# Optimization experiments

Hardware: AMD Instinct MI355X
Metric: run time of the kernel (lower is better)

## Reference

```python
import jax, jax.numpy as jnp
import numpy as np

BETA = 0.25


def setup_inputs() -> dict:
    key = jax.random.key(0)
    k1, k2 = jax.random.split(key)
    x = jax.random.normal(k1, (32, 64, 64, 64), dtype=jnp.float32)   # [B, C, H, W]
    emb = jax.random.normal(k2, (1024, 64), dtype=jnp.float32)       # [K, C] codebook
    return {"x": x, "emb": emb}


def reference(x, emb):
    b, c, h, w = x.shape
    # (b h w) c
    z = jnp.transpose(x, (0, 2, 3, 1)).reshape(-1, c)
    # squared euclidean distances (argmin identical to torch.cdist argmin)
    # ||z||^2 - 2 z e^T + ||e||^2, never taking sqrt since only argmin is used
    d = (jnp.sum(z * z, axis=1, keepdims=True)
         - 2.0 * jnp.einsum('nc,kc->nk', z, emb)
         + jnp.sum(emb * emb, axis=1)[None, :])        # [N, K]
    idx = jnp.argmin(d, axis=1)                        # [N] int
    e = emb[idx]                                       # gather [N, C]
    e = jnp.transpose(e.reshape(b, h, w, c), (0, 3, 1, 2))  # [B, C, H, W]
    codebook_loss = jnp.mean((jax.lax.stop_gradient(x) - e) ** 2)
    commitment_loss = BETA * jnp.mean((x - jax.lax.stop_gradient(e)) ** 2)
    loss = codebook_loss + commitment_loss
    o = x + jax.lax.stop_gradient(e - x)               # straight-through
    indices = idx.reshape(b, h, w)
    return (o, loss, indices)
```

## Files before the change

### kernel.cpp

```cpp
#include <hip/hip_runtime.h>

#define CCH     64
#define HW      4096
#define NPIX    131072
#define KCODES  1024
#define NELEM   (NPIX * CCH)
#define PPB     512
#define HALFK   512
#define MARGIN_Q 2u

typedef _Float16 f16;
typedef __attribute__((ext_vector_type(8))) _Float16 f16x8;
typedef __attribute__((ext_vector_type(4))) float    f32x4;

static __device__ __forceinline__ f32x4 mfma16(f16x8 a, f16x8 b, f32x4 c) {
    return __builtin_amdgcn_mfma_f32_16x16x32_f16(a, b, c, 0, 0, 0);
}
static __device__ __forceinline__ unsigned med3u(unsigned a, unsigned b, unsigned c) {
    unsigned d;
    asm("v_med3_u32 %0, %1, %2, %3" : "=v"(d) : "v"(a), "v"(b), "v"(c));
    return d;
}

__global__ __launch_bounds__(512, 2) void vq_fused(
    const float* __restrict__ x, const float* __restrict__ emb,
    float* __restrict__ o, float* __restrict__ idx_out,
    float* __restrict__ partial)
{
    __shared__ __align__(16) f16 cbH[HALFK * CCH];
    __shared__ __align__(16) f16 cbL[HALFK * CCH];
    __shared__ float eebl[HALFK];
    __shared__ unsigned buS[PPB];
    __shared__ float wred[8];

    const int t    = threadIdx.x;
    const int lane = t & 63;
    const int w    = t >> 6;
    const int col  = lane & 15;
    const int quad = lane >> 4;
    const int sw0  = 8 * (quad ^ (col & 7));
    const int sw1  = sw0 ^ 32;
    const int n0   = blockIdx.x * PPB;
    const int b    = n0 >> 12;
    const int p0   = n0 & 4095;
    const float* xb = x + (size_t)b * (CCH * HW) + p0;

    f16x8 aH[4][2], aL[4][2];
#pragma unroll
    for (int rt = 0; rt < 4; ++rt) {
        const int pp = w * 64 + rt * 16 + col;
#pragma unroll
        for (int kc = 0; kc < 2; ++kc) {
            f16x8 h, l;
#pragma unroll
            for (int j = 0; j < 8; ++j) {
                const int c = kc * 32 + quad * 8 + j;
                float zs = -2.0f * xb[(size_t)c * HW + pp];
                f16 hh = (f16)zs;
                h[j] = hh;
                l[j] = (f16)(zs - (float)hh);
            }
            aH[rt][kc] = h;
            aL[rt][kc] = l;
        }
    }

    unsigned best[16], best2[16];
#pragma unroll
    for (int s = 0; s < 16; ++s) { best[s] = 0xFFFFFFFFu; best2[s] = 0xFFFFFFFFu; }

    for (int half = 0; half < 2; ++half) {
        const int kbase = half * HALFK;
        {
            const float* src = emb + (size_t)(kbase + t) * CCH;
            float s = 0.f;
#pragma unroll
            for (int g = 0; g < 8; ++g) {
                float4 v0 = *(const float4*)(src + g * 8);
                float4 v1 = *(const float4*)(src + g * 8 + 4);
                float vv[8] = {v0.x, v0.y, v0.z, v0.w, v1.x, v1.y, v1.z, v1.w};
                f16x8 h, l;
#pragma unroll
                for (int j = 0; j < 8; ++j) {
                    f16 hh = (f16)vv[j];
                    h[j] = hh;
                    l[j] = (f16)(vv[j] - (float)hh);
                    s = fmaf(vv[j], vv[j], s);
                }
                const int off = t * 64 + 8 * (g ^ (t & 7));
                *(f16x8*)&cbH[off] = h;
                *(f16x8*)&cbL[off] = l;
            }
            eebl[t] = fmaf(s, 2048.0f, 1048576.0f);
        }
        __syncthreads();

#pragma unroll 4
        for (int tile = 0; tile < HALFK / 16; ++tile) {
            const int row = tile * 16 + col;
            const f16* bh = cbH + row * 64;
            const f16* bl = cbL + row * 64;
            f16x8 bH0 = *(const f16x8*)(bh + sw0);
            f16x8 bH1 = *(const f16x8*)(bh + sw1);
            f16x8 bL0 = *(const f16x8*)(bl + sw0);
            f16x8 bL1 = *(const f16x8*)(bl + sw1);
            const float eebc = eebl[row];
            const unsigned kb = (unsigned)(kbase + row);
#pragma unroll
            for (int rt = 0; rt < 4; ++rt) {
                f32x4 a4 = {0.f, 0.f, 0.f, 0.f};
                a4 = mfma16(aH[rt][0], bH0, a4);
                a4 = mfma16(aH[rt][1], bH1, a4);
                a4 = mfma16(aL[rt][0], bH0, a4);
                a4 = mfma16(aL[rt][1], bH1, a4);
                a4 = mfma16(aH[rt][0], bL0, a4);
                a4 = mfma16(aH[rt][1], bL1, a4);
#pragma unroll
                for (int r = 0; r < 4; ++r) {
                    float uf = fmaf(a4[r], 2048.0f, eebc);
                    unsigned pk = (((unsigned)uf) << 10) | kb;
                    const int s = rt * 4 + r;
                    best2[s] = med3u(pk, best[s], best2[s]);
                    best[s]  = min(best[s], pk);
                }
            }
        }
        __syncthreads();
    }

#pragma unroll
    for (int d = 1; d < 16; d <<= 1) {
#pragma unroll
        for (int s = 0; s < 16; ++s) {
            unsigned ob  = __shfl_xor(best[s],  d, 64);
            unsigned ob2 = __shfl_xor(best2[s], d, 64);
            best2[s] = med3u(best[s], ob, min(best2[s], ob2));
            best[s]  = min(best[s], ob);
        }
    }
    if (col == 0) {
#pragma unroll
        for (int rt = 0; rt < 4; ++rt)
#pragma unroll
            for (int r = 0; r < 4; ++r) {
                const int s = rt * 4 + r;
                const unsigned bb = best[s];
                const unsigned fl =
                    (((best2[s] >> 10) - (bb >> 10)) < MARGIN_Q) ? 0x80000000u : 0u;
                buS[w * 64 + rt * 16 + quad * 4 + r] = bb | fl;
            }
    }
    __syncthreads();

    const unsigned bu = buS[t];
    const unsigned bidx = bu & 1023u;
    idx_out[n0 + t] = (float)bidx;
    float ss = 0.f;
    {
        const float4* er4 = (const float4*)(emb + (size_t)bidx * CCH);
        const float* xbt = xb + t;
        float* ob = o + (size_t)b * (CCH * HW) + p0 + t;
#pragma unroll
        for (int i = 0; i < 16; ++i) {
            float4 ev = er4[i];
            float evv[4] = {ev.x, ev.y, ev.z, ev.w};
#pragma unroll
            for (int q = 0; q < 4; ++q) {
                const int c = i * 4 + q;
                float xv = xbt[(size_t)c * HW];
                float e  = evv[q];
                ob[(size_t)c * HW] = xv + (e - xv);
                float d = xv - e;
                ss = fmaf(d, d, ss);
            }
        }
    }
    for (int off = 32; off; off >>= 1) ss += __shfl_down(ss, off, 64);

    unsigned long long flags = __ballot((bu >> 31) != 0u);
    float extra = 0.f;
    while (flags) {
        const int m = __ffsll((long long)flags) - 1;
        flags &= flags - 1;
        const int pp2 = p0 + w * 64 + m;
        const int n   = n0 + w * 64 + m;
        const float zval = x[(size_t)b * (CCH * HW) + (size_t)lane * HW + pp2];
        float zf[CCH];
#pragma unroll
        for (int c = 0; c < CCH; ++c) zf[c] = __shfl(zval, c, 64);

        double bd = 1e300; int bi = 0;
        for (int j = 0; j < 16; ++j) {
            const int k = lane * 16 + j;
            const float4* er4 = (const float4*)(emb + (size_t)k * CCH);
            double d0 = 0.0, d1 = 0.0;
#pragma unroll
            for (int i = 0; i < 16; ++i) {
                float4 ev = er4[i];
                double t0 = (double)zf[i * 4 + 0] - (double)ev.x;
                double t1 = (double)zf[i * 4 + 1] - (double)ev.y;
                double t2 = (double)zf[i * 4 + 2] - (double)ev.z;
                double t3 = (double)zf[i * 4 + 3] - (double)ev.w;
                d0 = fma(t0, t0, d0); d1 = fma(t1, t1, d1);
                d0 = fma(t2, t2, d0); d1 = fma(t3, t3, d1);
            }
            double d = d0 + d1;
            if (d < bd) { bd = d; bi = k; }
        }
        for (int dlt = 1; dlt < 64; dlt <<= 1) {
            double od = __shfl_xor(bd, dlt, 64);
            int    oi = __shfl_xor(bi, dlt, 64);
            if (od < bd || (od == bd && oi < bi)) { bd = od; bi = oi; }
        }
        const int oldi = (int)(buS[w * 64 + m] & 1023u);
        if (bi != oldi) {
            if (lane == 0) idx_out[n] = (float)bi;
            const float xv = zval;
            const float eo = emb[(size_t)oldi * CCH + lane];
            const float en = emb[(size_t)bi   * CCH + lane];
            o[(size_t)b * (CCH * HW) + (size_t)lane * HW + pp2] = xv + (en - xv);
            const float dn = xv - en, dd = xv - eo;
            float delta = dn * dn - dd * dd;
            for (int off = 32; off; off >>= 1) delta += __shfl_down(delta, off, 64);
            extra += delta;
        }
    }

    if (lane == 0) wred[w] = ss + extra;
    __syncthreads();
    if (t == 0) {
        float tot = 0.f;
#pragma unroll
        for (int i = 0; i < 8; ++i) tot += wred[i];
        partial[blockIdx.x] = tot;
    }
}

__global__ void vq_fin(const float* __restrict__ partial, float* __restrict__ loss) {
    __shared__ float r[4];
    const int t = threadIdx.x, lane = t & 63, w = t >> 6;
    float s = partial[t];
    for (int off = 32; off; off >>= 1) s += __shfl_down(s, off, 64);
    if (lane == 0) r[w] = s;
    __syncthreads();
    if (t == 0) loss[0] = 1.25f * ((r[0] + r[1]) + (r[2] + r[3])) * (1.0f / (float)NELEM);
}

extern "C" void kernel_launch(void* const* d_in, const int* in_sizes, int n_in,
                              void* d_out, int out_size, void* d_ws, size_t ws_size,
                              hipStream_t stream) {
    const float* x   = (const float*)d_in[0];
    const float* emb = (const float*)d_in[1];
    float* out = (float*)d_out;
    float* wsf = (float*)d_ws;

    float* o_out    = out;
    float* loss_out = out + NELEM;
    float* idx_out  = out + NELEM + 1;

    vq_fused<<<NPIX / PPB, PPB, 0, stream>>>(x, emb, o_out, idx_out, wsf);
    vq_fin<<<1, 256, 0, stream>>>(wsf, loss_out);
}
```

Measured before the change: 177.8 us.

## Precompute split-f16 codebook once and stream it via double-buffered LDS DMA

A new prep kernel converts the codebook to hi/lo f16 halves and squared norms once in workspace. The main kernel no longer converts the codebook per block. It now handles 128 pixels per 256-thread block and streams 64-code chunks into double-buffered LDS with global_load_lds, so the loads overlap the MFMA work. This adds a kernel launch, more blocks and a per-chunk barrier. The med3 inline asm is replaced by min/max.

```diff
diff --git a/kernel.cpp b/kernel.cpp
--- a/kernel.cpp
+++ b/kernel.cpp
@@ -5,8 +5,8 @@
 #define NPIX    131072
 #define KCODES  1024
 #define NELEM   (NPIX * CCH)
-#define PPB     512
-#define HALFK   512
+#define PPB     128
+#define CK      64
 #define MARGIN_Q 2u
 
 typedef _Float16 f16;
@@ -16,22 +16,65 @@
 static __device__ __forceinline__ f32x4 mfma16(f16x8 a, f16x8 b, f32x4 c) {
     return __builtin_amdgcn_mfma_f32_16x16x32_f16(a, b, c, 0, 0, 0);
 }
-static __device__ __forceinline__ unsigned med3u(unsigned a, unsigned b, unsigned c) {
-    unsigned d;
-    asm("v_med3_u32 %0, %1, %2, %3" : "=v"(d) : "v"(a), "v"(b), "v"(c));
-    return d;
-}
-
-__global__ __launch_bounds__(512, 2) void vq_fused(
+static __device__ __forceinline__ void dma16(void* lds, const void* g) {
+    __builtin_amdgcn_global_load_lds(
+        (const __attribute__((address_space(1))) unsigned int*)g,
+        (__attribute__((address_space(3))) unsigned int*)lds, 16, 0, 0);
+}
+
+#define WS_EEB_F   64
+#define WS_CBH_B   8192
+#define WS_CBL_B   139264
+#define WS_PART_F  67584
+
+__global__ __launch_bounds__(256) void vq_prep(
+    const float* __restrict__ emb, f16* __restrict__ cbH, f16* __restrict__ cbL,
+    float* __restrict__ eeb_g)
+{
+    const int t = threadIdx.x;
+    if (blockIdx.x < 32) {
+        const int gid = blockIdx.x * 256 + t;
+        const int row = gid >> 3, gi = gid & 7;
+        const float* src = emb + (size_t)row * CCH + gi * 8;
+        float4 v0 = *(const float4*)(src);
+        float4 v1 = *(const float4*)(src + 4);
+        float vv[8] = {v0.x, v0.y, v0.z, v0.w, v1.x, v1.y, v1.z, v1.w};
+        f16x8 h, l;
+#pragma unroll
+        for (int j = 0; j < 8; ++j) {
+            f16 hh = (f16)vv[j];
+            h[j] = hh;
+            l[j] = (f16)(vv[j] - (float)hh);
+        }
+        const int off = row * 64 + 8 * (gi ^ (row & 7));
+        *(f16x8*)(cbH + off) = h;
+        *(f16x8*)(cbL + off) = l;
+    } else {
+        for (int r = t * 4; r < t * 4 + 4; ++r) {
+            const float4* row4 = (const float4*)(emb + (size_t)r * CCH);
+            float s = 0.f;
+#pragma unroll
+            for (int i = 0; i < 16; ++i) {
+                float4 v = row4[i];
+                s = fmaf(v.x, v.x, s); s = fmaf(v.y, v.y, s);
+                s = fmaf(v.z, v.z, s); s = fmaf(v.w, v.w, s);
+            }
+            eeb_g[r] = fmaf(s, 2048.0f, 1048576.0f);
+        }
+    }
+}
+
+__global__ __launch_bounds__(256, 4) void vq_fused(
     const float* __restrict__ x, const float* __restrict__ emb,
+    const f16* __restrict__ cbH, const f16* __restrict__ cbL,
+    const float* __restrict__ eeb_g,
     float* __restrict__ o, float* __restrict__ idx_out,
     float* __restrict__ partial)
 {
-    __shared__ __align__(16) f16 cbH[HALFK * CCH];
-    __shared__ __align__(16) f16 cbL[HALFK * CCH];
-    __shared__ float eebl[HALFK];
+    __shared__ __align__(16) char smem[32768];
+    __shared__ float eebl[2][CK];
     __shared__ unsigned buS[PPB];
-    __shared__ float wred[8];
+    __shared__ float wred[4];
 
     const int t    = threadIdx.x;
     const int lane = t & 63;
@@ -45,10 +88,26 @@
     const int p0   = n0 & 4095;
     const float* xb = x + (size_t)b * (CCH * HW) + p0;
 
-    f16x8 aH[4][2], aL[4][2];
-#pragma unroll
-    for (int rt = 0; rt < 4; ++rt) {
-        const int pp = w * 64 + rt * 16 + col;
+    auto stage = [&](int chunk, int bufi) {
+        const int k0 = chunk * CK;
+        char* lb = smem + bufi * 16384;
+        const char* gH = (const char*)cbH + (size_t)k0 * 128 + w * 2048 + lane * 16;
+        const char* gL = (const char*)cbL + (size_t)k0 * 128 + w * 2048 + lane * 16;
+        char* lH = lb + w * 2048;
+        char* lL = lb + 8192 + w * 2048;
+        dma16(lH,        gH);
+        dma16(lH + 1024, gH + 1024);
+        dma16(lL,        gL);
+        dma16(lL + 1024, gL + 1024);
+        if (t < CK) eebl[bufi][t] = eeb_g[k0 + t];
+    };
+
+    stage(0, 0);
+
+    f16x8 aH[2][2], aL[2][2];
+#pragma unroll
+    for (int rt = 0; rt < 2; ++rt) {
+        const int pp = w * 32 + rt * 16 + col;
 #pragma unroll
         for (int kc = 0; kc < 2; ++kc) {
             f16x8 h, l;
@@ -65,49 +124,31 @@
         }
     }
 
-    unsigned best[16], best2[16];
-#pragma unroll
-    for (int s = 0; s < 16; ++s) { best[s] = 0xFFFFFFFFu; best2[s] = 0xFFFFFFFFu; }
-
-    for (int half = 0; half < 2; ++half) {
-        const int kbase = half * HALFK;
-        {
-            const float* src = emb + (size_t)(kbase + t) * CCH;
-            float s = 0.f;
-#pragma unroll
-            for (int g = 0; g < 8; ++g) {
-                float4 v0 = *(const float4*)(src + g * 8);
-                float4 v1 = *(const float4*)(src + g * 8 + 4);
-                float vv[8] = {v0.x, v0.y, v0.z, v0.w, v1.x, v1.y, v1.z, v1.w};
-                f16x8 h, l;
-#pragma unroll
-                for (int j = 0; j < 8; ++j) {
-                    f16 hh = (f16)vv[j];
-                    h[j] = hh;
-                    l[j] = (f16)(vv[j] - (float)hh);
-                    s = fmaf(vv[j], vv[j], s);
-                }
-                const int off = t * 64 + 8 * (g ^ (t & 7));
-                *(f16x8*)&cbH[off] = h;
-                *(f16x8*)&cbL[off] = l;
-            }
-            eebl[t] = fmaf(s, 2048.0f, 1048576.0f);
-        }
+    unsigned best[8], best2[8];
+#pragma unroll
+    for (int s = 0; s < 8; ++s) { best[s] = 0xFFFFFFFFu; best2[s] = 0xFFFFFFFFu; }
+
+    for (int chunk = 0; chunk < KCODES / CK; ++chunk) {
+        const int cur = chunk & 1;
         __syncthreads();
-
-#pragma unroll 4
-        for (int tile = 0; tile < HALFK / 16; ++tile) {
-            const int row = tile * 16 + col;
-            const f16* bh = cbH + row * 64;
-            const f16* bl = cbL + row * 64;
+        if (chunk + 1 < KCODES / CK) stage(chunk + 1, cur ^ 1);
+
+        const f16* bufH = (const f16*)(smem + cur * 16384);
+        const f16* bufL = bufH + 4096;
+        const int k0 = chunk * CK;
+
+#pragma unroll
+        for (int tile = 0; tile < CK / 16; ++tile) {
+            const f16* bh = bufH + (tile * 16 + col) * 64;
+            const f16* bl = bufL + (tile * 16 + col) * 64;
             f16x8 bH0 = *(const f16x8*)(bh + sw0);
             f16x8 bH1 = *(const f16x8*)(bh + sw1);
             f16x8 bL0 = *(const f16x8*)(bl + sw0);
             f16x8 bL1 = *(const f16x8*)(bl + sw1);
-            const float eebc = eebl[row];
-            const unsigned kb = (unsigned)(kbase + row);
-#pragma unroll
-            for (int rt = 0; rt < 4; ++rt) {
+            const float eebc = eebl[cur][tile * 16 + col];
+            const unsigned kb = (unsigned)(k0 + tile * 16 + col);
+#pragma unroll
+            for (int rt = 0; rt < 2; ++rt) {
                 f32x4 a4 = {0.f, 0.f, 0.f, 0.f};
                 a4 = mfma16(aH[rt][0], bH0, a4);
                 a4 = mfma16(aH[rt][1], bH1, a4);
@@ -120,53 +161,53 @@
                     float uf = fmaf(a4[r], 2048.0f, eebc);
                     unsigned pk = (((unsigned)uf) << 10) | kb;
                     const int s = rt * 4 + r;
-                    best2[s] = med3u(pk, best[s], best2[s]);
+                    best2[s] = min(best2[s], max(pk, best[s]));
                     best[s]  = min(best[s], pk);
                 }
             }
         }
-        __syncthreads();
     }
 
 #pragma unroll
     for (int d = 1; d < 16; d <<= 1) {
 #pragma unroll
-        for (int s = 0; s < 16; ++s) {
+        for (int s = 0; s < 8; ++s) {
             unsigned ob  = __shfl_xor(best[s],  d, 64);
             unsigned ob2 = __shfl_xor(best2[s], d, 64);
-            best2[s] = med3u(best[s], ob, min(best2[s], ob2));
+            best2[s] = min(min(best2[s], ob2), max(best[s], ob));
             best[s]  = min(best[s], ob);
         }
     }
     if (col == 0) {
 #pragma unroll
-        for (int rt = 0; rt < 4; ++rt)
+        for (int rt = 0; rt < 2; ++rt)
 #pragma unroll
             for (int r = 0; r < 4; ++r) {
                 const int s = rt * 4 + r;
                 const unsigned bb = best[s];
                 const unsigned fl =
                     (((best2[s] >> 10) - (bb >> 10)) < MARGIN_Q) ? 0x80000000u : 0u;
-                buS[w * 64 + rt * 16 + quad * 4 + r] = bb | fl;
+                buS[w * 32 + rt * 16 + quad * 4 + r] = bb | fl;
             }
     }
     __syncthreads();
 
-    const unsigned bu = buS[t];
-    const unsigned bidx = bu & 1023u;
-    idx_out[n0 + t] = (float)bidx;
     float ss = 0.f;
     {
-        const float4* er4 = (const float4*)(emb + (size_t)bidx * CCH);
-        const float* xbt = xb + t;
-        float* ob = o + (size_t)b * (CCH * HW) + p0 + t;
-#pragma unroll
-        for (int i = 0; i < 16; ++i) {
+        const int pl = t & 127;
+        const int cs = (t >> 7) * 32;
+        const unsigned bidx = buS[pl] & 1023u;
+        if ((t >> 7) == 0) idx_out[n0 + pl] = (float)bidx;
+        const float4* er4 = (const float4*)(emb + (size_t)bidx * CCH + cs);
+        const float* xbt = xb + pl;
+        float* ob = o + (size_t)b * (CCH * HW) + p0 + pl;
+#pragma unroll
+        for (int i = 0; i < 8; ++i) {
             float4 ev = er4[i];
             float evv[4] = {ev.x, ev.y, ev.z, ev.w};
 #pragma unroll
             for (int q = 0; q < 4; ++q) {
-                const int c = i * 4 + q;
+                const int c = cs + i * 4 + q;
                 float xv = xbt[(size_t)c * HW];
                 float e  = evv[q];
                 ob[(size_t)c * HW] = xv + (e - xv);
@@ -177,13 +218,14 @@
     }
     for (int off = 32; off; off >>= 1) ss += __shfl_down(ss, off, 64);
 
-    unsigned long long flags = __ballot((bu >> 31) != 0u);
+    unsigned long long flags =
+        __ballot((lane < 32) && ((buS[w * 32 + lane] >> 31) != 0u));
     float extra = 0.f;
     while (flags) {
         const int m = __ffsll((long long)flags) - 1;
         flags &= flags - 1;
-        const int pp2 = p0 + w * 64 + m;
-        const int n   = n0 + w * 64 + m;
+        const int pp2 = p0 + w * 32 + m;
+        const int n   = n0 + w * 32 + m;
         const float zval = x[(size_t)b * (CCH * HW) + (size_t)lane * HW + pp2];
         float zf[CCH];
 #pragma unroll
@@ -212,7 +254,7 @@
             int    oi = __shfl_xor(bi, dlt, 64);
             if (od < bd || (od == bd && oi < bi)) { bd = od; bi = oi; }
         }
-        const int oldi = (int)(buS[w * 64 + m] & 1023u);
+        const int oldi = (int)(buS[w * 32 + m] & 1023u);
         if (bi != oldi) {
             if (lane == 0) idx_out[n] = (float)bi;
             const float xv = zval;
@@ -228,18 +270,14 @@
 
     if (lane == 0) wred[w] = ss + extra;
     __syncthreads();
-    if (t == 0) {
-        float tot = 0.f;
-#pragma unroll
-        for (int i = 0; i < 8; ++i) tot += wred[i];
-        partial[blockIdx.x] = tot;
-    }
+    if (t == 0)
+        partial[blockIdx.x] = (wred[0] + wred[1]) + (wred[2] + wred[3]);
 }
 
 __global__ void vq_fin(const float* __restrict__ partial, float* __restrict__ loss) {
     __shared__ float r[4];
     const int t = threadIdx.x, lane = t & 63, w = t >> 6;
-    float s = partial[t];
+    float s = partial[t] + partial[256 + t] + partial[512 + t] + partial[768 + t];
     for (int off = 32; off; off >>= 1) s += __shfl_down(s, off, 64);
     if (lane == 0) r[w] = s;
     __syncthreads();
@@ -253,11 +291,18 @@
     const float* emb = (const float*)d_in[1];
     float* out = (float*)d_out;
     float* wsf = (float*)d_ws;
+    char*  wsb = (char*)d_ws;
 
     float* o_out    = out;
     float* loss_out = out + NELEM;
     float* idx_out  = out + NELEM + 1;
-
-    vq_fused<<<NPIX / PPB, PPB, 0, stream>>>(x, emb, o_out, idx_out, wsf);
-    vq_fin<<<1, 256, 0, stream>>>(wsf, loss_out);
-}
+    float* eeb_g    = wsf + WS_EEB_F;
+    f16*   cbH      = (f16*)(wsb + WS_CBH_B);
+    f16*   cbL      = (f16*)(wsb + WS_CBL_B);
+    float* part     = wsf + WS_PART_F;
+
+    vq_prep<<<33, 256, 0, stream>>>(emb, cbH, cbL, eeb_g);
+    vq_fused<<<NPIX / PPB, 256, 0, stream>>>(x, emb, cbH, cbL, eeb_g,
+                                             o_out, idx_out, part);
+    vq_fin<<<1, 256, 0, stream>>>(part, loss_out);
+}
```

Result: slower. 235.7 us (+32.6%).
